# Kernel optimization log

Measured on AMD Instinct MI355X. Metric: run time of the kernel, lower is better.

The kernel has to match this reference:

```python
import jax, jax.numpy as jnp
import numpy as np

S, B, D, H, E, K, DF = 1024, 16, 512, 8, 16, 2, 2048
HD = D // H
EPS = 1e-5


def _layernorm(x, g, b):
    m = x.mean(-1, keepdims=True)
    v = ((x - m) ** 2).mean(-1, keepdims=True)
    return (x - m) / jnp.sqrt(v + EPS) * g + b


def setup_inputs() -> dict:
    key = jax.random.key(0)
    ks = jax.random.split(key, 10)
    s = 0.02
    return {
        "src": jax.random.normal(ks[0], (S, B, D), jnp.float32),
        "pos": jax.random.normal(ks[1], (S, B, D), jnp.float32),
        "in_proj_w": jax.random.normal(ks[2], (3 * D, D), jnp.float32) * s,
        "in_proj_b": jnp.zeros((3 * D,), jnp.float32),
        "out_w": jax.random.normal(ks[3], (D, D), jnp.float32) * s,
        "out_b": jnp.zeros((D,), jnp.float32),
        "norm1_g": jnp.ones((D,), jnp.float32),
        "norm1_b": jnp.zeros((D,), jnp.float32),
        "gate_w": jax.random.normal(ks[4], (E, D), jnp.float32) * s,
        "gate_b": jnp.zeros((E,), jnp.float32),
        "w1": jax.random.normal(ks[5], (E, DF, D), jnp.float32) * s,
        "b1": jnp.zeros((E, DF), jnp.float32),
        "w2": jax.random.normal(ks[6], (E, D, DF), jnp.float32) * s,
        "b2": jnp.zeros((E, D), jnp.float32),
    }


def reference(src, pos, in_proj_w, in_proj_b, out_w, out_b, norm1_g, norm1_b,
              gate_w, gate_b, w1, b1, w2, b2):
    # ---- self attention (torch nn.MultiheadAttention, seq-first) ----
    qk_in = src + pos                      # q = k = src + pos, v = src
    wq, wk, wv = jnp.split(in_proj_w, 3, axis=0)
    bq, bk, bv = jnp.split(in_proj_b, 3, axis=0)
    q = qk_in @ wq.T + bq                  # [S,B,D]
    k = qk_in @ wk.T + bk
    v = src @ wv.T + bv

    def heads(x):                          # [S,B,D] -> [B,H,S,HD]
        return x.reshape(S, B, H, HD).transpose(1, 2, 0, 3)

    qh, kh, vh = heads(q), heads(k), heads(v)
    scores = jnp.einsum('bhqd,bhkd->bhqk', qh * (1.0 / np.sqrt(HD)), kh)
    attn = jax.nn.softmax(scores, axis=-1)
    o = jnp.einsum('bhqk,bhkd->bhqd', attn, vh)
    o = o.transpose(2, 0, 1, 3).reshape(S, B, D) @ out_w.T + out_b

    x = _layernorm(src + o, norm1_g, norm1_b)  # post-norm residual

    # ---- MoE FFN (FMoE NaiveGate, top-k=2, no capacity drop) ----
    t = x.reshape(S * B, D)                # tokens
    logits = t @ gate_w.T + gate_b         # [T,E]
    topv, topi = jax.lax.top_k(logits, K)  # [T,K]
    gate_score = jax.nn.softmax(topv, axis=-1)
    T = S * B
    comb = jnp.zeros((T, E), t.dtype).at[jnp.arange(T)[:, None], topi].add(gate_score)

    def body(acc, packed):
        W1, B1, W2, B2, c = packed         # per-expert weights + combine col [T]
        h = jax.nn.relu(t @ W1.T + B1)     # [T,DF]
        y = h @ W2.T + B2                  # [T,D]
        return acc + c[:, None] * y, None

    acc, _ = jax.lax.scan(body, jnp.zeros_like(t), (w1, b1, w2, b2, comb.T))
    # pre_lnorm=False branch: output = inp + core_out (internal LN unused)
    return x + acc.reshape(S, B, D)
```

## Files before the change

### kernel.cpp

```cpp
#include <hip/hip_runtime.h>
#include <hip/hip_bf16.h>

typedef float f4 __attribute__((ext_vector_type(4)));
typedef float f32x4 __attribute__((ext_vector_type(4)));
typedef short short8 __attribute__((ext_vector_type(8)));
typedef unsigned short u16x4 __attribute__((ext_vector_type(4)));
typedef unsigned short u16x8 __attribute__((ext_vector_type(8)));
typedef unsigned int u32x4 __attribute__((ext_vector_type(4)));
typedef unsigned int u32x8 __attribute__((ext_vector_type(8)));

#define S_LEN 1024
#define BATCH 16
#define DIM   512
#define NH    8
#define HDIM  64
#define NE    16
#define DFF   2048
#define T_TOK 16384
#define CAP   34816
#define BM    128

__device__ __forceinline__ unsigned short f2bf(float f) {
  union { float f; unsigned u; } v; v.f = f;
  unsigned r = v.u + 0x7fffu + ((v.u >> 16) & 1u);
  return (unsigned short)(r >> 16);
}
__device__ __forceinline__ float bf2f(unsigned short h) {
  union { unsigned u; float f; } v; v.u = ((unsigned)h) << 16;
  return v.f;
}

__device__ __forceinline__ void load_lds16(const void* g, void* l) {
  __builtin_amdgcn_global_load_lds(
      (__attribute__((address_space(1))) void*)(void*)g,
      (__attribute__((address_space(3))) void*)l, 16, 0, 0);
}

__device__ __forceinline__ short8 pack_hi8(const unsigned* val) {
  union { unsigned u[4]; short8 s; } t;
#pragma unroll
  for (int i = 0; i < 4; i++)
    t.u[i] = (val[2 * i] >> 16) | (val[2 * i + 1] & 0xFFFF0000u);
  return t.s;
}
__device__ __forceinline__ short8 pack_lo8(const unsigned* val) {
  union { unsigned u[4]; short8 s; } t;
#pragma unroll
  for (int i = 0; i < 4; i++)
    t.u[i] = (val[2 * i] & 0xFFFFu) | (val[2 * i + 1] << 16);
  return t.s;
}

__global__ __launch_bounds__(256) void k_cvt_bf16(const float* __restrict__ in,
                                                  unsigned short* __restrict__ outb,
                                                  size_t n) {
  size_t i = ((size_t)blockIdx.x * 256 + threadIdx.x) * 4;
  size_t stride = (size_t)gridDim.x * 1024;
  for (; i < n; i += stride) {
    f4 v = *(const f4*)&in[i];
    u16x4 o;
    o[0] = f2bf(v[0]); o[1] = f2bf(v[1]); o[2] = f2bf(v[2]); o[3] = f2bf(v[3]);
    *(u16x4*)&outb[i] = o;
  }
}

__global__ __launch_bounds__(256) void k_split_w(const float* __restrict__ in,
                                                 unsigned short* __restrict__ hi,
                                                 unsigned short* __restrict__ lo,
                                                 size_t n) {
  size_t i = ((size_t)blockIdx.x * 256 + threadIdx.x) * 4;
  size_t stride = (size_t)gridDim.x * 1024;
  for (; i < n; i += stride) {
    f4 v = *(const f4*)&in[i];
    u16x4 h, l;
#pragma unroll
    for (int j = 0; j < 4; j++) {
      unsigned short hh = f2bf(v[j]);
      h[j] = hh;
      l[j] = f2bf(v[j] - bf2f(hh));
    }
    *(u16x4*)&hi[i] = h;
    *(u16x4*)&lo[i] = l;
  }
}

__global__ __launch_bounds__(256) void k_init(int* __restrict__ slotTok,
                                              float* __restrict__ slotW,
                                              int* __restrict__ counts) {
  int i = blockIdx.x * 256 + threadIdx.x;
  if (i < CAP) { slotTok[i] = -1; slotW[i] = 0.f; }
  if (i < NE) counts[i] = 0;
}

__global__ __launch_bounds__(256) void k_zero_pad(const int* __restrict__ counts,
                                                  const int* __restrict__ off_pad,
                                                  unsigned short* __restrict__ Xg) {
  const int e = blockIdx.x;
  const int start = off_pad[e] + counts[e];
  const int end = off_pad[e + 1];
  for (int row = start; row < end; row++)
    *(unsigned int*)&Xg[(size_t)row * DIM + threadIdx.x * 2] = 0u;
}

__global__ __launch_bounds__(256, 2) void k_gemm_split(
    const float* __restrict__ A, const float* __restrict__ A2,
    const unsigned short* __restrict__ Wh, const unsigned short* __restrict__ Wl,
    const float* __restrict__ bias, int epi,
    unsigned* __restrict__ p0, unsigned* __restrict__ p1) {
  __shared__ unsigned short AhL[128 * 32];
  __shared__ unsigned short AlL[128 * 32];
  __shared__ unsigned short WhL[128 * 32];
  __shared__ unsigned short WlL[128 * 32];
  const int tid = threadIdx.x, lane = tid & 63, wid = tid >> 6;
  const int wm = wid >> 1, wn = wid & 1;
  const int m0 = blockIdx.x * 128, n0 = blockIdx.y * 128;
  const int row = tid >> 1, half = tid & 1;
  const int xr = (row >> 1) & 3;
  f32x4 acc[4][4] = {};
  f4 ar[4];
#pragma unroll
  for (int j = 0; j < 4; j++) {
    const size_t aoff = (size_t)(m0 + row) * 512 + half * 16 + j * 4;
    ar[j] = *(const f4*)&A[aoff];
    if (A2) { f4 v2 = *(const f4*)&A2[aoff]; ar[j] += v2; }
  }
  for (int k0 = 0; k0 < 512; k0 += 32) {
    __syncthreads();
    u16x8 hi8[2], lo8[2];
#pragma unroll
    for (int j = 0; j < 16; j++) {
      const float x = ar[j >> 2][j & 3];
      const unsigned short h = f2bf(x);
      hi8[j >> 3][j & 7] = h;
      lo8[j >> 3][j & 7] = f2bf(x - bf2f(h));
    }
    const int c0 = half * 2;
    *(u16x8*)&AhL[row * 32 + (((c0 + 0) ^ xr) << 3)] = hi8[0];
    *(u16x8*)&AhL[row * 32 + (((c0 + 1) ^ xr) << 3)] = hi8[1];
    *(u16x8*)&AlL[row * 32 + (((c0 + 0) ^ xr) << 3)] = lo8[0];
    *(u16x8*)&AlL[row * 32 + (((c0 + 1) ^ xr) << 3)] = lo8[1];
#pragma unroll
    for (int i = 0; i < 2; i++) {
      const int rowW = i * 64 + wid * 16 + (lane >> 2);
      const int clog = (lane & 3) ^ ((rowW >> 1) & 3);
      const size_t woff = (size_t)(n0 + rowW) * 512 + k0 + (clog << 3);
      load_lds16(Wh + woff, &WhL[i * 2048 + wid * 512]);
      load_lds16(Wl + woff, &WlL[i * 2048 + wid * 512]);
    }
    __syncthreads();
    if (k0 + 32 < 512) {
#pragma unroll
      for (int j = 0; j < 4; j++) {
        const size_t aoff = (size_t)(m0 + row) * 512 + k0 + 32 + half * 16 + j * 4;
        ar[j] = *(const f4*)&A[aoff];
        if (A2) { f4 v2 = *(const f4*)&A2[aoff]; ar[j] += v2; }
      }
    }
    const int l15 = lane & 15, lk = lane >> 4;
    const int xa = (l15 >> 1) & 3;
    short8 avh[4], avl[4], bvh[4], bvl[4];
#pragma unroll
    for (int mi = 0; mi < 4; mi++) {
      const int mr = wm * 64 + mi * 16 + l15;
      avh[mi] = *(const short8*)&AhL[mr * 32 + ((lk ^ xa) << 3)];
      avl[mi] = *(const short8*)&AlL[mr * 32 + ((lk ^ xa) << 3)];
    }
#pragma unroll
    for (int ni = 0; ni < 4; ni++) {
      const int nr = wn * 64 + ni * 16 + l15;
      bvh[ni] = *(const short8*)&WhL[nr * 32 + ((lk ^ xa) << 3)];
      bvl[ni] = *(const short8*)&WlL[nr * 32 + ((lk ^ xa) << 3)];
    }
#pragma unroll
    for (int mi = 0; mi < 4; mi++) {
#pragma unroll
      for (int ni = 0; ni < 4; ni++) {
        acc[mi][ni] = __builtin_amdgcn_mfma_f32_16x16x32_bf16(avh[mi], bvh[ni], acc[mi][ni], 0, 0, 0);
        acc[mi][ni] = __builtin_amdgcn_mfma_f32_16x16x32_bf16(avh[mi], bvl[ni], acc[mi][ni], 0, 0, 0);
        acc[mi][ni] = __builtin_amdgcn_mfma_f32_16x16x32_bf16(avl[mi], bvh[ni], acc[mi][ni], 0, 0, 0);
      }
    }
  }
#pragma unroll
  for (int mi = 0; mi < 4; mi++) {
    const int rb = m0 + wm * 64 + mi * 16 + ((lane >> 4) << 2);
#pragma unroll
    for (int ni = 0; ni < 4; ni++) {
      const int n = n0 + wn * 64 + ni * 16 + (lane & 15);
      const float bn = bias[n];
#pragma unroll
      for (int r = 0; r < 4; r++) {
        const int m = rb + r;
        const int bidx = m & 15, ss = m >> 4;
        float v = acc[mi][ni][r] + bn;
        unsigned* pl;
        int nn;
        if (epi == 0) {
          if (n < 512) { v *= 0.125f; pl = p0; nn = n; }
          else { pl = p1; nn = n - 512; }
        } else { pl = p0; nn = n; }
        const size_t off = ((size_t)(bidx * NH + (nn >> 6)) * S_LEN + ss) * HDIM + (nn & 63);
        const unsigned short hh = f2bf(v);
        pl[off] = ((unsigned)hh << 16) | (unsigned)f2bf(v - bf2f(hh));
      }
    }
  }
}

__global__ __launch_bounds__(256, 3) void k_gemm_f32(
    const float* __restrict__ A, const float* __restrict__ W,
    const float* __restrict__ bias, int K,
    float* __restrict__ o0) {
  __shared__ float Alt[32][132];
  __shared__ float Wlt[32][132];
  const int tid = threadIdx.x, tx = tid & 15, ty = tid >> 4;
  const int m0 = blockIdx.x * 128, n0 = blockIdx.y * 128;
  float acc[8][8];
#pragma unroll
  for (int i = 0; i < 8; i++) {
#pragma unroll
    for (int j = 0; j < 8; j++) acc[i][j] = 0.f;
  }
  f4 ar[4], wr[4];
#pragma unroll
  for (int i = 0; i < 4; i++) {
    const int c = tid + i * 256;
    const int r = c >> 3, j = (c & 7) * 4;
    ar[i] = *(const f4*)&A[(size_t)(m0 + r) * K + j];
    wr[i] = *(const f4*)&W[(size_t)(n0 + r) * K + j];
  }
  for (int k0 = 0; k0 < K; k0 += 32) {
    __syncthreads();
#pragma unroll
    for (int i = 0; i < 4; i++) {
      const int c = tid + i * 256;
      const int r = c >> 3, j = (c & 7) * 4;
      Alt[j + 0][r] = ar[i][0]; Alt[j + 1][r] = ar[i][1];
      Alt[j + 2][r] = ar[i][2]; Alt[j + 3][r] = ar[i][3];
      Wlt[j + 0][r] = wr[i][0]; Wlt[j + 1][r] = wr[i][1];
      Wlt[j + 2][r] = wr[i][2]; Wlt[j + 3][r] = wr[i][3];
    }
    __syncthreads();
    if (k0 + 32 < K) {
#pragma unroll
      for (int i = 0; i < 4; i++) {
        const int c = tid + i * 256;
        const int r = c >> 3, j = (c & 7) * 4;
        ar[i] = *(const f4*)&A[(size_t)(m0 + r) * K + k0 + 32 + j];
        wr[i] = *(const f4*)&W[(size_t)(n0 + r) * K + k0 + 32 + j];
      }
    }
#pragma unroll 4
    for (int kk = 0; kk < 32; kk++) {
      float a[8], w8[8];
      *(f4*)&a[0]  = *(const f4*)&Alt[kk][ty * 8];
      *(f4*)&a[4]  = *(const f4*)&Alt[kk][ty * 8 + 4];
      *(f4*)&w8[0] = *(const f4*)&Wlt[kk][tx * 8];
      *(f4*)&w8[4] = *(const f4*)&Wlt[kk][tx * 8 + 4];
#pragma unroll
      for (int mi = 0; mi < 8; mi++) {
#pragma unroll
        for (int ni = 0; ni < 8; ni++)
          acc[mi][ni] = fmaf(a[mi], w8[ni], acc[mi][ni]);
      }
    }
  }
#pragma unroll
  for (int mi = 0; mi < 8; mi++) {
    const size_t m = (size_t)(m0 + ty * 8 + mi);
#pragma unroll
    for (int nj = 0; nj < 2; nj++) {
      const int n = n0 + tx * 8 + nj * 4;
      f4 v;
      v[0] = acc[mi][nj * 4 + 0] + bias[n + 0];
      v[1] = acc[mi][nj * 4 + 1] + bias[n + 1];
      v[2] = acc[mi][nj * 4 + 2] + bias[n + 2];
      v[3] = acc[mi][nj * 4 + 3] + bias[n + 3];
      *(f4*)&o0[m * 512 + n] = v;
    }
  }
}

__global__ __launch_bounds__(256, 3) void k_attn(
    const unsigned* __restrict__ Qp, const unsigned* __restrict__ Kp,
    const unsigned* __restrict__ Vp, float* __restrict__ O) {
  const int q0 = blockIdx.x * 64;
  const int bh = blockIdx.y;
  const int b = bh >> 3, h = bh & 7;
  const size_t base = (size_t)bh * (S_LEN * HDIM);
  __shared__ unsigned KL[64][68];
  __shared__ unsigned VL[64][68];
  const int tid = threadIdx.x, lane = tid & 63, w = tid >> 6;
  const int l15 = lane & 15, lq = lane >> 4;
  const int srcA = l15 + 16 * ((2 * lq) & 3);
  const int srcB = l15 + 16 * ((2 * lq + 1) & 3);
  const bool selHi = (lane & 32) != 0;
  short8 qh[2], ql[2];
  {
    const size_t qoff = base + (size_t)(q0 + 16 * w + l15) * HDIM + lq * 8;
    u32x8 qv0 = *(const u32x8*)&Qp[qoff];
    u32x8 qv1 = *(const u32x8*)&Qp[qoff + 32];
    qh[0] = pack_hi8((const unsigned*)&qv0); ql[0] = pack_lo8((const unsigned*)&qv0);
    qh[1] = pack_hi8((const unsigned*)&qv1); ql[1] = pack_lo8((const unsigned*)&qv1);
  }
  const int sr = tid >> 2, sq = (tid & 3) * 16;
  const int jq = tid & 3;
  u32x4 kr[4], vr[4];
  {
    const size_t ko = base + (size_t)sr * HDIM + sq;
#pragma unroll
    for (int i = 0; i < 4; i++) {
      kr[i] = *(const u32x4*)&Kp[ko + 4 * i];
      vr[i] = *(const u32x4*)&Vp[ko + 4 * i];
    }
  }
  float m_ = -1e30f, l_ = 0.f;
  f32x4 acc[4] = {};

  for (int kt = 0; kt < 16; kt++) {
#pragma unroll
    for (int i = 0; i < 4; i++) *(u32x4*)&KL[sr][sq + 4 * i] = kr[i];
#pragma unroll
    for (int j = 0; j < 16; j++) {
      const int jj = j ^ jq;
      VL[sq + jj][sr] = vr[jj >> 2][jj & 3];
    }
    __syncthreads();
    if (kt < 15) {
      const size_t ko = base + (size_t)((kt + 1) * 64 + sr) * HDIM + sq;
#pragma unroll
      for (int i = 0; i < 4; i++) {
        kr[i] = *(const u32x4*)&Kp[ko + 4 * i];
        vr[i] = *(const u32x4*)&Vp[ko + 4 * i];
      }
    }
    f32x4 sc[4] = {};
#pragma unroll
    for (int c = 0; c < 2; c++) {
      short8 kfh[4], kfl[4];
#pragma unroll
      for (int n = 0; n < 4; n++) {
        u32x8 k32 = *(const u32x8*)&KL[16 * n + l15][c * 32 + lq * 8];
        kfh[n] = pack_hi8((const unsigned*)&k32);
        kfl[n] = pack_lo8((const unsigned*)&k32);
      }
#pragma unroll
      for (int n = 0; n < 4; n++) {
        sc[n] = __builtin_amdgcn_mfma_f32_16x16x32_bf16(kfh[n], qh[c], sc[n], 0, 0, 0);
        sc[n] = __builtin_amdgcn_mfma_f32_16x16x32_bf16(kfl[n], qh[c], sc[n], 0, 0, 0);
        sc[n] = __builtin_amdgcn_mfma_f32_16x16x32_bf16(kfh[n], ql[c], sc[n], 0, 0, 0);
      }
    }
    float tm = fmaxf(fmaxf(fmaxf(sc[0][0], sc[0][1]), fmaxf(sc[0][2], sc[0][3])),
                     fmaxf(fmaxf(sc[1][0], sc[1][1]), fmaxf(sc[1][2], sc[1][3])));
    tm = fmaxf(tm, fmaxf(fmaxf(fmaxf(sc[2][0], sc[2][1]), fmaxf(sc[2][2], sc[2][3])),
                         fmaxf(fmaxf(sc[3][0], sc[3][1]), fmaxf(sc[3][2], sc[3][3]))));
    tm = fmaxf(tm, __shfl_xor(tm, 16));
    tm = fmaxf(tm, __shfl_xor(tm, 32));
    const float mn = fmaxf(m_, tm);
    const float esc = __expf(m_ - mn);
    m_ = mn;
    float rs = 0.f;
    unsigned pk[4][4];
#pragma unroll
    for (int n = 0; n < 4; n++) {
#pragma unroll
      for (int r = 0; r < 4; r++) {
        const float p = __expf(sc[n][r] - mn);
        rs += p;
        const unsigned short hh = f2bf(p);
        pk[n][r] = ((unsigned)hh << 16) | (unsigned)f2bf(p - bf2f(hh));
      }
    }
    rs += __shfl_xor(rs, 16);
    rs += __shfl_xor(rs, 32);
    l_ = l_ * esc + rs;
    float escR[4];
#pragma unroll
    for (int r = 0; r < 4; r++) escR[r] = __shfl(esc, 4 * lq + r);
#pragma unroll
    for (int n = 0; n < 4; n++) {
#pragma unroll
      for (int r = 0; r < 4; r++) acc[n][r] *= escR[r];
    }
#pragma unroll
    for (int c = 0; c < 2; c++) {
      unsigned val[8];
#pragma unroll
      for (int j = 0; j < 8; j++) {
        const int src = (j >> 2) ? srcB : srcA;
        const unsigned sA = (unsigned)__shfl((int)pk[2 * c + 0][j & 3], src);
        const unsigned sB = (unsigned)__shfl((int)pk[2 * c + 1][j & 3], src);
        val[j] = selHi ? sB : sA;
      }
      const short8 ph = pack_hi8(val);
      const short8 plo = pack_lo8(val);
      short8 vfh[4], vfl[4];
#pragma unroll
      for (int n = 0; n < 4; n++) {
        u32x8 v32 = *(const u32x8*)&VL[16 * n + l15][c * 32 + lq * 8];
        vfh[n] = pack_hi8((const unsigned*)&v32);
        vfl[n] = pack_lo8((const unsigned*)&v32);
      }
#pragma unroll
      for (int n = 0; n < 4; n++) {
        acc[n] = __builtin_amdgcn_mfma_f32_16x16x32_bf16(ph, vfh[n], acc[n], 0, 0, 0);
        acc[n] = __builtin_amdgcn_mfma_f32_16x16x32_bf16(ph, vfl[n], acc[n], 0, 0, 0);
        acc[n] = __builtin_amdgcn_mfma_f32_16x16x32_bf16(plo, vfh[n], acc[n], 0, 0, 0);
      }
    }
    __syncthreads();
  }
  const float inv = 1.f / l_;
  float invR[4];
#pragma unroll
  for (int r = 0; r < 4; r++) invR[r] = __shfl(inv, 4 * lq + r);
#pragma unroll
  for (int r = 0; r < 4; r++) {
    const int srow = q0 + 16 * w + 4 * lq + r;
    float* orow = &O[((size_t)srow * BATCH + b) * DIM + h * HDIM];
#pragma unroll
    for (int n = 0; n < 4; n++) orow[16 * n + l15] = acc[n][r] * invR[r];
  }
}

__global__ __launch_bounds__(256) void k_ln(const float* __restrict__ src,
                                            const float* __restrict__ proj,
                                            const float* __restrict__ g,
                                            const float* __restrict__ bt,
                                            float* __restrict__ xout) {
  const int wid = threadIdx.x >> 6, lane = threadIdx.x & 63;
  const int tok = blockIdx.x * 4 + wid;
  const size_t base = (size_t)tok * DIM + lane * 8;
  f4 a0 = *(const f4*)&src[base],  a1 = *(const f4*)&src[base + 4];
  f4 p0 = *(const f4*)&proj[base], p1 = *(const f4*)&proj[base + 4];
  float x[8];
  x[0] = a0[0] + p0[0]; x[1] = a0[1] + p0[1]; x[2] = a0[2] + p0[2]; x[3] = a0[3] + p0[3];
  x[4] = a1[0] + p1[0]; x[5] = a1[1] + p1[1]; x[6] = a1[2] + p1[2]; x[7] = a1[3] + p1[3];
  float s = 0.f, sq = 0.f;
#pragma unroll
  for (int j = 0; j < 8; j++) { s += x[j]; sq = fmaf(x[j], x[j], sq); }
#pragma unroll
  for (int d = 1; d < 64; d <<= 1) { s += __shfl_xor(s, d); sq += __shfl_xor(sq, d); }
  const float mean = s * (1.f / 512.f);
  const float var = sq * (1.f / 512.f) - mean * mean;
  const float rstd = 1.f / sqrtf(var + 1e-5f);
  const int ci = lane * 8;
  f4 o0v, o1v;
#pragma unroll
  for (int j = 0; j < 4; j++) o0v[j] = (x[j] - mean) * rstd * g[ci + j] + bt[ci + j];
#pragma unroll
  for (int j = 0; j < 4; j++) o1v[j] = (x[4 + j] - mean) * rstd * g[ci + 4 + j] + bt[ci + 4 + j];
  *(f4*)&xout[base] = o0v;
  *(f4*)&xout[base + 4] = o1v;
}

__global__ __launch_bounds__(256) void k_gate(const float* __restrict__ x,
                                              const float* __restrict__ gw,
                                              const float* __restrict__ gb,
                                              int* __restrict__ topi,
                                              float* __restrict__ topw,
                                              int* __restrict__ counts) {
  __shared__ float xs[16 * 520];
  __shared__ int hist[16];
  const int tid = threadIdx.x;
  const int tl = tid >> 4, e = tid & 15;
  if (tid < 16) hist[tid] = 0;
  const float gbe = gb[e];
  const float* wrow = gw + (size_t)e * DIM;
  for (int tile = 0; tile < 4; tile++) {
    const int t0 = blockIdx.x * 64 + tile * 16;
    __syncthreads();
    {
      const int r = tid >> 4, cbase = (tid & 15) * 32;
#pragma unroll
      for (int j = 0; j < 8; j++) {
        const int c = cbase + j * 4;
        const int ch = c >> 2;
        const int pc = ch ^ ((ch >> 3) & 7);
        *(f4*)&xs[r * 520 + pc * 4] = *(const f4*)&x[(size_t)(t0 + r) * DIM + c];
      }
    }
    __syncthreads();
    float d = gbe;
#pragma unroll 8
    for (int c = 0; c < DIM; c += 4) {
      const int ch = c >> 2;
      const int pc = ch ^ ((ch >> 3) & 7);
      f4 xv = *(const f4*)&xs[tl * 520 + pc * 4];
      f4 wv = *(const f4*)&wrow[c];
      d = fmaf(xv[0], wv[0], d); d = fmaf(xv[1], wv[1], d);
      d = fmaf(xv[2], wv[2], d); d = fmaf(xv[3], wv[3], d);
    }
    float v1 = d, v2 = -1e30f;
    int i1 = e, i2 = 1000;
#pragma unroll
    for (int s = 1; s < 16; s <<= 1) {
      const float ov1 = __shfl_xor(v1, s), ov2 = __shfl_xor(v2, s);
      const int oi1 = __shfl_xor(i1, s), oi2 = __shfl_xor(i2, s);
      if (ov1 > v1 || (ov1 == v1 && oi1 < i1)) {
        float nv2; int ni2;
        if (v1 > ov2 || (v1 == ov2 && i1 < oi2)) { nv2 = v1; ni2 = i1; }
        else { nv2 = ov2; ni2 = oi2; }
        v1 = ov1; i1 = oi1; v2 = nv2; i2 = ni2;
      } else if (ov1 > v2 || (ov1 == v2 && oi1 < i2)) {
        v2 = ov1; i2 = oi1;
      }
    }
    if (e == 0) {
      const int t = t0 + tl;
      const float e1 = __expf(v2 - v1);
      const float inv = 1.f / (1.f + e1);
      topi[2 * t] = i1;  topi[2 * t + 1] = i2;
      topw[2 * t] = inv; topw[2 * t + 1] = e1 * inv;
      atomicAdd(&hist[i1], 1);
      atomicAdd(&hist[i2], 1);
    }
  }
  __syncthreads();
  if (tid < 16 && hist[tid] > 0) atomicAdd(&counts[tid], hist[tid]);
}

__global__ void k_offsets(const int* __restrict__ counts,
                          int* __restrict__ off_pad, int* __restrict__ cursor) {
  if (threadIdx.x == 0) {
    int o = 0;
    off_pad[0] = 0;
    for (int e = 0; e < NE; e++) {
      cursor[e] = 0;
      o += ((counts[e] + BM - 1) / BM) * BM;
      off_pad[e + 1] = o;
    }
  }
}

__global__ __launch_bounds__(256) void k_scatter(const float* __restrict__ x,
                                                 const int* __restrict__ topi,
                                                 const float* __restrict__ topw,
                                                 const int* __restrict__ off_pad,
                                                 int* __restrict__ cursor,
                                                 int* __restrict__ slotTok,
                                                 float* __restrict__ slotW,
                                                 unsigned short* __restrict__ Xg) {
  __shared__ int lcnt[16];
  __shared__ int gbase[16];
  __shared__ int posArr[128];
  const int tid = threadIdx.x;
  const int a0 = blockIdx.x * 128;
  if (tid < 16) lcnt[tid] = 0;
  __syncthreads();
  if (tid < 128) {
    const int a = a0 + tid;
    const int e = topi[a];
    const int lrank = atomicAdd(&lcnt[e], 1);
    posArr[tid] = (e << 24) | lrank;
  }
  __syncthreads();
  if (tid < 16) {
    const int c = lcnt[tid];
    gbase[tid] = (c > 0) ? atomicAdd(&cursor[tid], c) : 0;
  }
  __syncthreads();
  if (tid < 128) {
    const int a = a0 + tid;
    const int pk = posArr[tid];
    const int e = pk >> 24, lrank = pk & 0xffffff;
    const int pos = off_pad[e] + gbase[e] + lrank;
    posArr[tid] = pos;
    slotTok[pos] = a >> 1;
    slotW[pos] = topw[a];
  }
  __syncthreads();
  const int w = tid >> 6, lane = tid & 63;
#pragma unroll 4
  for (int i = 0; i < 32; i++) {
    const int idx = w * 32 + i;
    const int pos = posArr[idx];
    const int tok = (a0 + idx) >> 1;
    const size_t sb = (size_t)tok * DIM + lane * 8;
    f4 v0 = *(const f4*)&x[sb], v1 = *(const f4*)&x[sb + 4];
    u16x8 hh;
    hh[0] = f2bf(v0[0]); hh[1] = f2bf(v0[1]); hh[2] = f2bf(v0[2]); hh[3] = f2bf(v0[3]);
    hh[4] = f2bf(v1[0]); hh[5] = f2bf(v1[1]); hh[6] = f2bf(v1[2]); hh[7] = f2bf(v1[3]);
    *(u16x8*)&Xg[(size_t)pos * DIM + lane * 8] = hh;
  }
}

__global__ __launch_bounds__(256) void k_gemm_bf16(
    const unsigned short* __restrict__ A, int lda,
    const unsigned short* __restrict__ Wb, size_t westride, int ldw, int wrow0,
    const float* __restrict__ bias, int bstride, int brow0,
    int K, int epi,
    unsigned short* __restrict__ Hout, int ldh,
    float* __restrict__ dout,
    const int* __restrict__ slotTok, const float* __restrict__ slotW,
    const int* __restrict__ off_pad) {
  int bx = blockIdx.x;
  const int nwg = gridDim.x;
  if ((nwg & 7) == 0) bx = (bx & 7) * (nwg >> 3) + (bx >> 3);
  const int m0 = bx * BM;
  if (m0 >= off_pad[NE]) return;
  int e = 0;
  while (off_pad[e + 1] <= m0) e++;
  const unsigned short* W = Wb + (size_t)e * westride;
  const int n0 = blockIdx.y * 128;
  __shared__ unsigned short Al[128 * 64];
  __shared__ unsigned short Bl[128 * 64];
  const int tid = threadIdx.x, lane = tid & 63, wid = tid >> 6;
  const int wm = wid >> 1, wn = wid & 1;
  f32x4 acc[4][4] = {};
  const int srow = wid * 32 + (lane >> 3);
  const int scol = (((lane & 7) ^ ((lane >> 3) & 7)) << 3);
  for (int k0 = 0; k0 < K; k0 += 64) {
    const unsigned short* ga = A + (size_t)(m0 + srow) * lda + k0 + scol;
    const unsigned short* gw = W + (size_t)(wrow0 + n0 + srow) * ldw + k0 + scol;
#pragma unroll
    for (int i = 0; i < 4; i++) {
      load_lds16(ga + (size_t)i * 8 * lda, &Al[(wid * 32 + i * 8) * 64]);
      load_lds16(gw + (size_t)i * 8 * ldw, &Bl[(wid * 32 + i * 8) * 64]);
    }
    __syncthreads();
#pragma unroll
    for (int kk = 0; kk < 2; kk++) {
      short8 av[4], bv[4];
      const int ckx = (kk * 4 + (lane >> 4)) ^ (lane & 7);
#pragma unroll
      for (int mi = 0; mi < 4; mi++)
        av[mi] = *(const short8*)&Al[(wm * 64 + mi * 16 + (lane & 15)) * 64 + ckx * 8];
#pragma unroll
      for (int ni = 0; ni < 4; ni++)
        bv[ni] = *(const short8*)&Bl[(wn * 64 + ni * 16 + (lane & 15)) * 64 + ckx * 8];
#pragma unroll
      for (int mi = 0; mi < 4; mi++) {
#pragma unroll
        for (int ni = 0; ni < 4; ni++)
          acc[mi][ni] = __builtin_amdgcn_mfma_f32_16x16x32_bf16(av[mi], bv[ni], acc[mi][ni], 0, 0, 0);
      }
    }
    __syncthreads();
  }
#pragma unroll
  for (int mi = 0; mi < 4; mi++) {
    const int rb = m0 + wm * 64 + mi * 16 + ((lane >> 4) << 2);
#pragma unroll
    for (int ni = 0; ni < 4; ni++) {
      const int n = n0 + wn * 64 + ni * 16 + (lane & 15);
      const float bn = bias ? bias[(size_t)e * bstride + brow0 + n] : 0.f;
      if (epi == 0) {
#pragma unroll
        for (int r = 0; r < 4; r++) {
          float v = acc[mi][ni][r] + bn;
          v = fmaxf(v, 0.f);
          Hout[(size_t)(rb + r) * ldh + n] = f2bf(v);
        }
      } else {
#pragma unroll
        for (int r = 0; r < 4; r++) {
          const int tok = slotTok[rb + r];
          if (tok >= 0) {
            const float v = (acc[mi][ni][r] + bn) * slotW[rb + r];
            atomicAdd(&dout[(size_t)tok * DIM + n], v);
          }
        }
      }
    }
  }
}

extern "C" void kernel_launch(void* const* d_in, const int* in_sizes, int n_in,
                              void* d_out, int out_size, void* d_ws, size_t ws_size,
                              hipStream_t stream) {
  const float* src       = (const float*)d_in[0];
  const float* pos       = (const float*)d_in[1];
  const float* in_proj_w = (const float*)d_in[2];
  const float* in_proj_b = (const float*)d_in[3];
  const float* out_w     = (const float*)d_in[4];
  const float* out_b     = (const float*)d_in[5];
  const float* norm1_g   = (const float*)d_in[6];
  const float* norm1_b   = (const float*)d_in[7];
  const float* gate_w    = (const float*)d_in[8];
  const float* gate_b    = (const float*)d_in[9];
  const float* w1        = (const float*)d_in[10];
  const float* b1        = (const float*)d_in[11];
  const float* w2        = (const float*)d_in[12];
  const float* b2        = (const float*)d_in[13];
  float* out = (float*)d_out;
  char* wsb = (char*)d_ws;

  unsigned* Qp = (unsigned*)(wsb + 0);
  unsigned* Kp = (unsigned*)(wsb + 33554432);
  unsigned* Vp = (unsigned*)(wsb + 67108864);
  float* ob = (float*)(wsb + 100663296);
  float* proj = (float*)(wsb + 0);
  unsigned short* w1b = (unsigned short*)(wsb + 0);
  unsigned short* w2b = (unsigned short*)(wsb + 33554432);
  unsigned short* Xg  = (unsigned short*)(wsb + 67108864);
  unsigned short* Hb  = (unsigned short*)(wsb + 102760448);
  unsigned short* wih = (unsigned short*)(wsb + 134217728);
  unsigned short* wil = (unsigned short*)(wsb + 135790592);
  char* smallb = wsb + 174063616;
  int*   topi    = (int*)  (smallb + 0);
  float* topw    = (float*)(smallb + 131072);
  int*   slotTok = (int*)  (smallb + 262144);
  float* slotW   = (float*)(smallb + 401408);
  int*   counts  = (int*)  (smallb + 540672);
  int*   off_pad = (int*)  (smallb + 540736);
  int*   cursor  = (int*)  (smallb + 540864);

  k_init<<<(CAP + 255) / 256, 256, 0, stream>>>(slotTok, slotW, counts);
  k_split_w<<<768, 256, 0, stream>>>(in_proj_w, wih, wil, (size_t)1536 * 512);
  k_gemm_split<<<dim3(128, 8), 256, 0, stream>>>(src, pos, wih, wil, in_proj_b, 0, Qp, Kp);
  k_gemm_split<<<dim3(128, 4), 256, 0, stream>>>(src, nullptr, wih + (size_t)1024 * 512,
                                                 wil + (size_t)1024 * 512, in_proj_b + 1024,
                                                 1, Vp, nullptr);
  k_attn<<<dim3(16, 128), 256, 0, stream>>>(Qp, Kp, Vp, ob);
  k_cvt_bf16<<<2048, 256, 0, stream>>>(w2, w2b, (size_t)NE * DIM * DFF);
  k_gemm_f32<<<dim3(128, 4), 256, 0, stream>>>(ob, out_w, out_b, 512, proj);
  k_ln<<<4096, 256, 0, stream>>>(src, proj, norm1_g, norm1_b, out);
  k_cvt_bf16<<<2048, 256, 0, stream>>>(w1, w1b, (size_t)NE * DFF * DIM);
  k_gate<<<T_TOK / 64, 256, 0, stream>>>(out, gate_w, gate_b, topi, topw, counts);
  k_offsets<<<1, 64, 0, stream>>>(counts, off_pad, cursor);
  k_zero_pad<<<NE, 256, 0, stream>>>(counts, off_pad, Xg);
  k_scatter<<<256, 256, 0, stream>>>(out, topi, topw, off_pad, cursor, slotTok, slotW, Xg);
  for (int p = 0; p < 2; ++p) {
    k_gemm_bf16<<<dim3(CAP / BM, 8), 256, 0, stream>>>(
        Xg, DIM, w1b, (size_t)DFF * DIM, DIM, p * 1024,
        b1, DFF, p * 1024, DIM, 0, Hb, 1024,
        nullptr, nullptr, nullptr, off_pad);
    k_gemm_bf16<<<dim3(CAP / BM, 4), 256, 0, stream>>>(
        Hb, 1024, w2b + (size_t)p * 1024, (size_t)DIM * DFF, DFF, 0,
        (p == 0 ? b2 : nullptr), DIM, 0, 1024, 1, nullptr, 0,
        out, slotTok, slotW, off_pad);
  }
}
```

Baseline: 985.2 us.

## Store V transposed from projection GEMM and pre-split K/V hi/lo in attention LDS

The QKV projection epilogue for V (epi!=0) now stages results through a shared-memory bounce buffer and writes V transposed as [b,h,d,s], so attention can load V rows with contiguous vector loads. This replaces the per-element transposing scatter into LDS. The attention kernel also splits K and V into separate bf16 hi/lo LDS arrays once per tile, so the MMA operand loads no longer repack 32-bit pairs each iteration. Occupancy hint is raised from 3 to 4 blocks. The cost is extra syncs and LDS traffic in the GEMM epilogue and a changed V layout contract between the two kernels.

```diff
diff --git a/kernel.cpp b/kernel.cpp
--- a/kernel.cpp
+++ b/kernel.cpp
@@ -107,10 +107,12 @@
     const unsigned short* __restrict__ Wh, const unsigned short* __restrict__ Wl,
     const float* __restrict__ bias, int epi,
     unsigned* __restrict__ p0, unsigned* __restrict__ p1) {
-  __shared__ unsigned short AhL[128 * 32];
-  __shared__ unsigned short AlL[128 * 32];
-  __shared__ unsigned short WhL[128 * 32];
-  __shared__ unsigned short WlL[128 * 32];
+  __shared__ __align__(16) char smem[33792];
+  unsigned short* AhL = (unsigned short*)smem;
+  unsigned short* AlL = (unsigned short*)(smem + 8192);
+  unsigned short* WhL = (unsigned short*)(smem + 16384);
+  unsigned short* WlL = (unsigned short*)(smem + 24576);
+  unsigned* bounce = (unsigned*)smem;
   const int tid = threadIdx.x, lane = tid & 63, wid = tid >> 6;
   const int wm = wid >> 1, wn = wid & 1;
   const int m0 = blockIdx.x * 128, n0 = blockIdx.y * 128;
@@ -181,27 +183,64 @@
       }
     }
   }
-#pragma unroll
-  for (int mi = 0; mi < 4; mi++) {
-    const int rb = m0 + wm * 64 + mi * 16 + ((lane >> 4) << 2);
-#pragma unroll
-    for (int ni = 0; ni < 4; ni++) {
-      const int n = n0 + wn * 64 + ni * 16 + (lane & 15);
-      const float bn = bias[n];
-#pragma unroll
-      for (int r = 0; r < 4; r++) {
-        const int m = rb + r;
-        const int bidx = m & 15, ss = m >> 4;
-        float v = acc[mi][ni][r] + bn;
-        unsigned* pl;
-        int nn;
-        if (epi == 0) {
+  const int l15 = lane & 15, lq = lane >> 4;
+  if (epi == 0) {
+#pragma unroll
+    for (int mi = 0; mi < 4; mi++) {
+      const int rb = m0 + wm * 64 + mi * 16 + (lq << 2);
+#pragma unroll
+      for (int ni = 0; ni < 4; ni++) {
+        const int n = n0 + wn * 64 + ni * 16 + l15;
+        const float bn = bias[n];
+#pragma unroll
+        for (int r = 0; r < 4; r++) {
+          const int m = rb + r;
+          const int bidx = m & 15, ss = m >> 4;
+          float v = acc[mi][ni][r] + bn;
+          unsigned* pl;
+          int nn;
           if (n < 512) { v *= 0.125f; pl = p0; nn = n; }
           else { pl = p1; nn = n - 512; }
-        } else { pl = p0; nn = n; }
-        const size_t off = ((size_t)(bidx * NH + (nn >> 6)) * S_LEN + ss) * HDIM + (nn & 63);
-        const unsigned short hh = f2bf(v);
-        pl[off] = ((unsigned)hh << 16) | (unsigned)f2bf(v - bf2f(hh));
+          const size_t off = ((size_t)(bidx * NH + (nn >> 6)) * S_LEN + ss) * HDIM + (nn & 63);
+          const unsigned short hh = f2bf(v);
+          pl[off] = ((unsigned)hh << 16) | (unsigned)f2bf(v - bf2f(hh));
+        }
+      }
+    }
+  } else {
+    const int s_base = m0 >> 4;
+    for (int halfn = 0; halfn < 2; halfn++) {
+      __syncthreads();
+      if (wn == halfn) {
+#pragma unroll
+        for (int mi = 0; mi < 4; mi++) {
+          const int mlb = wm * 64 + mi * 16 + (lq << 2);
+#pragma unroll
+          for (int ni = 0; ni < 4; ni++) {
+            const int n = n0 + wn * 64 + ni * 16 + l15;
+            const float bn = bias[n];
+            const int nc = ni * 16 + l15;
+#pragma unroll
+            for (int r = 0; r < 4; r++) {
+              const float v = acc[mi][ni][r] + bn;
+              const unsigned short hh = f2bf(v);
+              bounce[(mlb + r) * 66 + nc] =
+                  ((unsigned)hh << 16) | (unsigned)f2bf(v - bf2f(hh));
+            }
+          }
+        }
+      }
+      __syncthreads();
+#pragma unroll
+      for (int i = 0; i < 4; i++) {
+        const int idx = tid + 256 * i;
+        const int nc = idx & 63, bb = idx >> 6;
+        const int ng = n0 + halfn * 64 + nc;
+        const int hh_ = ng >> 6, dd = ng & 63;
+        u32x8 vals;
+#pragma unroll
+        for (int s = 0; s < 8; s++) vals[s] = bounce[(s * 16 + bb) * 66 + nc];
+        *(u32x8*)&p0[((size_t)(bb * NH + hh_) * HDIM + dd) * S_LEN + s_base] = vals;
       }
     }
   }
@@ -281,15 +320,15 @@
   }
 }
 
-__global__ __launch_bounds__(256, 3) void k_attn(
+__global__ __launch_bounds__(256, 4) void k_attn(
     const unsigned* __restrict__ Qp, const unsigned* __restrict__ Kp,
     const unsigned* __restrict__ Vp, float* __restrict__ O) {
   const int q0 = blockIdx.x * 64;
   const int bh = blockIdx.y;
   const int b = bh >> 3, h = bh & 7;
   const size_t base = (size_t)bh * (S_LEN * HDIM);
-  __shared__ unsigned KL[64][68];
-  __shared__ unsigned VL[64][68];
+  __shared__ unsigned short KhL[64][72], KlL[64][72];
+  __shared__ unsigned short VhL[64][72], VlL[64][72];
   const int tid = threadIdx.x, lane = tid & 63, w = tid >> 6;
   const int l15 = lane & 15, lq = lane >> 4;
   const int srcA = l15 + 16 * ((2 * lq) & 3);
@@ -304,34 +343,41 @@
     qh[1] = pack_hi8((const unsigned*)&qv1); ql[1] = pack_lo8((const unsigned*)&qv1);
   }
   const int sr = tid >> 2, sq = (tid & 3) * 16;
-  const int jq = tid & 3;
   u32x4 kr[4], vr[4];
   {
     const size_t ko = base + (size_t)sr * HDIM + sq;
+    const size_t vo = base + (size_t)sr * S_LEN + sq;
 #pragma unroll
     for (int i = 0; i < 4; i++) {
       kr[i] = *(const u32x4*)&Kp[ko + 4 * i];
-      vr[i] = *(const u32x4*)&Vp[ko + 4 * i];
+      vr[i] = *(const u32x4*)&Vp[vo + 4 * i];
     }
   }
   float m_ = -1e30f, l_ = 0.f;
   f32x4 acc[4] = {};
 
   for (int kt = 0; kt < 16; kt++) {
-#pragma unroll
-    for (int i = 0; i < 4; i++) *(u32x4*)&KL[sr][sq + 4 * i] = kr[i];
-#pragma unroll
-    for (int j = 0; j < 16; j++) {
-      const int jj = j ^ jq;
-      VL[sq + jj][sr] = vr[jj >> 2][jj & 3];
+    {
+      const unsigned* ku = (const unsigned*)kr;
+      const unsigned* vu = (const unsigned*)vr;
+      *(short8*)&KhL[sr][sq + 0] = pack_hi8(ku);
+      *(short8*)&KhL[sr][sq + 8] = pack_hi8(ku + 8);
+      *(short8*)&KlL[sr][sq + 0] = pack_lo8(ku);
+      *(short8*)&KlL[sr][sq + 8] = pack_lo8(ku + 8);
+      *(short8*)&VhL[sr][sq + 0] = pack_hi8(vu);
+      *(short8*)&VhL[sr][sq + 8] = pack_hi8(vu + 8);
+      *(short8*)&VlL[sr][sq + 0] = pack_lo8(vu);
+      *(short8*)&VlL[sr][sq + 8] = pack_lo8(vu + 8);
     }
     __syncthreads();
     if (kt < 15) {
-      const size_t ko = base + (size_t)((kt + 1) * 64 + sr) * HDIM + sq;
+      const int s0n = (kt + 1) * 64;
+      const size_t ko = base + (size_t)(s0n + sr) * HDIM + sq;
+      const size_t vo = base + (size_t)sr * S_LEN + s0n + sq;
 #pragma unroll
       for (int i = 0; i < 4; i++) {
         kr[i] = *(const u32x4*)&Kp[ko + 4 * i];
-        vr[i] = *(const u32x4*)&Vp[ko + 4 * i];
+        vr[i] = *(const u32x4*)&Vp[vo + 4 * i];
       }
     }
     f32x4 sc[4] = {};
@@ -340,9 +386,8 @@
       short8 kfh[4], kfl[4];
 #pragma unroll
       for (int n = 0; n < 4; n++) {
-        u32x8 k32 = *(const u32x8*)&KL[16 * n + l15][c * 32 + lq * 8];
-        kfh[n] = pack_hi8((const unsigned*)&k32);
-        kfl[n] = pack_lo8((const unsigned*)&k32);
+        kfh[n] = *(const short8*)&KhL[16 * n + l15][c * 32 + lq * 8];
+        kfl[n] = *(const short8*)&KlL[16 * n + l15][c * 32 + lq * 8];
       }
 #pragma unroll
       for (int n = 0; n < 4; n++) {
@@ -398,9 +443,8 @@
       short8 vfh[4], vfl[4];
 #pragma unroll
       for (int n = 0; n < 4; n++) {
-        u32x8 v32 = *(const u32x8*)&VL[16 * n + l15][c * 32 + lq * 8];
-        vfh[n] = pack_hi8((const unsigned*)&v32);
-        vfl[n] = pack_lo8((const unsigned*)&v32);
+        vfh[n] = *(const short8*)&VhL[16 * n + l15][c * 32 + lq * 8];
+        vfl[n] = *(const short8*)&VlL[16 * n + l15][c * 32 + lq * 8];
       }
 #pragma unroll
       for (int n = 0; n < 4; n++) {
```

New measurement: 962.9 us. 2.3% less time.
